# Kernel optimization log

Hardware: AMD Instinct MI355X
Metric: run time of the kernel (lower is better)

## Reference

```python
import jax, jax.numpy as jnp
import numpy as np

H = 512  # hidden_dimension
B = 32
S = 2048


def setup_inputs() -> dict:
    key = jax.random.key(0)
    k1, k2, k3, k4, k5, k6 = jax.random.split(key, 6)
    decoder_hide = jax.random.normal(k1, (B, H), dtype=jnp.float32)
    encoder_out = jax.random.normal(k2, (B, S, 2 * H), dtype=jnp.float32)
    mask = jax.random.randint(k3, (B, S), 0, 2, dtype=jnp.int32)
    bound = 1.0 / np.sqrt(3 * H)
    W_attn = jax.random.uniform(k4, (3 * H, H), minval=-bound, maxval=bound, dtype=jnp.float32)
    b_attn = jax.random.uniform(k5, (H,), minval=-bound, maxval=bound, dtype=jnp.float32)
    bound_v = 1.0 / np.sqrt(H)
    v_w = jax.random.uniform(k6, (H,), minval=-bound_v, maxval=bound_v, dtype=jnp.float32)
    return {"decoder_hide": decoder_hide, "encoder_out": encoder_out, "mask": mask,
            "W_attn": W_attn, "b_attn": b_attn, "v_w": v_w}


def reference(decoder_hide, encoder_out, mask, W_attn, b_attn, v_w):
    # Split the concat-linear: cat((h, enc)) @ W == h @ W[:H] + enc @ W[H:]
    W_h = W_attn[:H]        # [H, H]
    W_e = W_attn[H:]        # [2H, H]
    dec_proj = decoder_hide @ W_h + b_attn                 # [B, H]
    enc_proj = jnp.einsum('bse,eh->bsh', encoder_out, W_e)  # [B, S, H]
    energy = jnp.tanh(enc_proj + dec_proj[:, None, :])      # [B, S, H]
    attention = jnp.einsum('bsh,h->bs', energy, v_w)        # [B, S]
    attention = jnp.where(mask == 0, jnp.float32(-100000.0), attention)
    return jax.nn.softmax(attention, axis=1)
```

## Files before the change

### kernel.cpp

```cpp
#include <hip/hip_runtime.h>
#include <hip/hip_bf16.h>
#include <math.h>

#define Hdim 512
#define Bdim 32
#define Sdim 2048
#define Kdim 1024
#define Mtot (Bdim * Sdim)

#define RGROWS 64
#define HK 512
#define NSTEP 8
#define RGPB 4

typedef __attribute__((ext_vector_type(8))) short short8;
typedef __attribute__((ext_vector_type(4))) float floatx4;

__device__ __forceinline__ short f2bf(float f) {
    union { float f; unsigned u; } v; v.f = f;
    unsigned r = v.u + 0x7fffu + ((v.u >> 16) & 1u);
    return (short)(r >> 16);
}

__device__ __forceinline__ short8 cvt8(float4 a, float4 b) {
    union { short8 s; __hip_bfloat162 h[4]; } u;
    u.h[0] = __float22bfloat162_rn(make_float2(a.x, a.y));
    u.h[1] = __float22bfloat162_rn(make_float2(a.z, a.w));
    u.h[2] = __float22bfloat162_rn(make_float2(b.x, b.y));
    u.h[3] = __float22bfloat162_rn(make_float2(b.z, b.w));
    return u.s;
}

__device__ __forceinline__ float fast_tanh(float x) {
    float ax = fabsf(x);
    float e  = __expf(-2.0f * ax);
    float r  = (1.0f - e) * __builtin_amdgcn_rcpf(1.0f + e);
    return copysignf(r, x);
}

__global__ __launch_bounds__(256) void prep_kernel(
    const float* __restrict__ W_attn, const float* __restrict__ dec,
    const float* __restrict__ b_attn, short* __restrict__ Wbp,
    float* __restrict__ dec_proj)
{
    const int t = threadIdx.x;
    if (blockIdx.x < 512) {
        const float* We = W_attn + Hdim * Hdim;
        __shared__ short tile[32][33];
        const int k0 = (blockIdx.x >> 4) * 32;
        const int n0 = (blockIdx.x & 15) * 32;
        const int r = t >> 5, c = t & 31;
        #pragma unroll
        for (int rr = 0; rr < 4; ++rr)
            tile[r + rr * 8][c] = f2bf(We[(size_t)(k0 + r + rr * 8) * Hdim + n0 + c]);
        __syncthreads();
        if (t < 128) {
            const int n_loc = t >> 2;
            const int q     = t & 3;
            const int nt    = (n0 + n_loc) >> 4;
            const int lnn   = (n0 + n_loc) & 15;
            const int ks    = k0 >> 5;
            short8 v;
            #pragma unroll
            for (int r2 = 0; r2 < 8; ++r2) v[r2] = tile[q * 8 + r2][n_loc];
            ((short8*)Wbp)[((nt * 32 + ks) * 64) + q * 16 + lnn] = v;
        }
    } else {
        __shared__ float partl[2][128];
        const int bid = blockIdx.x - 512;
        const int b  = bid >> 2;
        const int cb = bid & 3;
        const int c  = cb * 128 + (t & 127);
        const int kh = t >> 7;
        float acc = 0.0f;
        const int kbeg = kh * 256, kend = kbeg + 256;
        #pragma unroll 8
        for (int k = kbeg; k < kend; ++k)
            acc = fmaf(dec[b * Hdim + k], W_attn[(size_t)k * Hdim + c], acc);
        partl[kh][t & 127] = acc;
        __syncthreads();
        if (t < 128)
            dec_proj[b * Hdim + cb * 128 + t] = partl[0][t] + partl[1][t] + b_attn[cb * 128 + t];
    }
}

__global__ __launch_bounds__(512, 2) void scores_kernel(
    const float* __restrict__ enc,
    const short* __restrict__ Wbp,
    const float* __restrict__ dec_proj,
    const float* __restrict__ v_w,
    float* __restrict__ scores)
{
    __shared__ __align__(16) short Abuf[2][RGROWS * HK];
    __shared__ float redl[RGROWS][9];

    const int t    = threadIdx.x;
    const int w    = t >> 6;
    const int lane = t & 63;
    const int ln   = lane & 15;
    const int quad = lane >> 4;

    const int b = blockIdx.x >> 3;
    const float* Ablk = enc + (size_t)blockIdx.x * (RGPB * RGROWS) * Kdim;

    const int pf0 = (quad ^ (ln & 7)) * 8;
    const int pf1 = pf0 ^ 32;

    const short8* Bp = ((const short8*)Wbp) + lane;

    float dpv[4], vwv[4];
    #pragma unroll
    for (int j = 0; j < 4; ++j) {
        const int col = w * 64 + j * 16 + ln;
        dpv[j] = dec_proj[b * Hdim + col];
        vwv[j] = v_w[col];
    }

    floatx4 acc[4][4];
    #pragma unroll
    for (int i = 0; i < 4; ++i)
        #pragma unroll
        for (int j = 0; j < 4; ++j)
            acc[i][j] = (floatx4)(0.0f);

    float4 stage[16];

    #define ISSUE(hh) do {                                                    \
        const float* p_ = Ablk + (size_t)((hh) >> 1) * RGROWS * Kdim          \
                         + ((hh) & 1) * HK + lane * 8;                        \
        _Pragma("unroll")                                                     \
        for (int j_ = 0; j_ < 8; ++j_) {                                      \
            const float4* g_ = (const float4*)(p_ + (size_t)(j_ * 8 + w) * Kdim); \
            stage[2 * j_]     = g_[0];                                        \
            stage[2 * j_ + 1] = g_[1];                                        \
        }                                                                     \
    } while (0)

    #define WRITEHALF(bi_) do {                                               \
        _Pragma("unroll")                                                     \
        for (int j_ = 0; j_ < 8; ++j_) {                                      \
            const int r_ = j_ * 8 + w;                                        \
            *(short8*)&Abuf[bi_][r_ * HK + ((lane ^ (r_ & 7)) << 3)] =        \
                cvt8(stage[2 * j_], stage[2 * j_ + 1]);                       \
        }                                                                     \
    } while (0)

    ISSUE(0);
    WRITEHALF(0);
    __syncthreads();

    #pragma unroll 1
    for (int h = 0; h < 2 * RGPB; ++h) {
        const int bi  = h & 1;
        const short* Ab = Abuf[bi];
        const int ksb = (h & 1) * 16;

        #pragma unroll
        for (int s = 0; s < NSTEP; ++s) {
            const int ks = ksb + 2 * s;
            short8 b0[4], b1[4];
            #pragma unroll
            for (int j = 0; j < 4; ++j)
                b0[j] = Bp[((size_t)(w * 4 + j) * 32 + ks) * 64];
            #pragma unroll
            for (int j = 0; j < 4; ++j)
                b1[j] = Bp[((size_t)(w * 4 + j) * 32 + ks + 1) * 64];

            if (s == 3 && h < 2 * RGPB - 1) ISSUE(h + 1);

            short8 af[4];
            #pragma unroll
            for (int i2 = 0; i2 < 4; ++i2)
                af[i2] = *(const short8*)&Ab[(i2 * 16 + ln) * HK + s * 64 + pf0];
            #pragma unroll
            for (int i2 = 0; i2 < 4; ++i2)
                #pragma unroll
                for (int j = 0; j < 4; ++j)
                    acc[i2][j] = __builtin_amdgcn_mfma_f32_16x16x32_bf16(
                                     af[i2], b0[j], acc[i2][j], 0, 0, 0);
            #pragma unroll
            for (int i2 = 0; i2 < 4; ++i2)
                af[i2] = *(const short8*)&Ab[(i2 * 16 + ln) * HK + s * 64 + pf1];
            #pragma unroll
            for (int i2 = 0; i2 < 4; ++i2)
                #pragma unroll
                for (int j = 0; j < 4; ++j)
                    acc[i2][j] = __builtin_amdgcn_mfma_f32_16x16x32_bf16(
                                     af[i2], b1[j], acc[i2][j], 0, 0, 0);
        }

        if (h & 1) {
            const int rg = h >> 1;
            #pragma unroll
            for (int i2 = 0; i2 < 4; ++i2) {
                #pragma unroll
                for (int reg = 0; reg < 4; ++reg) {
                    float s2 = 0.0f;
                    #pragma unroll
                    for (int j = 0; j < 4; ++j) {
                        float x = acc[i2][j][reg] + dpv[j];
                        s2 = fmaf(vwv[j], fast_tanh(x), s2);
                    }
                    s2 += __shfl_xor(s2, 1, 64);
                    s2 += __shfl_xor(s2, 2, 64);
                    s2 += __shfl_xor(s2, 4, 64);
                    s2 += __shfl_xor(s2, 8, 64);
                    if (ln == 0)
                        redl[i2 * 16 + quad * 4 + reg][w] = s2;
                }
            }
            __syncthreads();
            if (t < RGROWS) {
                float s2 = 0.0f;
                #pragma unroll
                for (int wv = 0; wv < 8; ++wv) s2 += redl[t][wv];
                scores[blockIdx.x * (RGPB * RGROWS) + rg * RGROWS + t] = s2;
            }
            #pragma unroll
            for (int i = 0; i < 4; ++i)
                #pragma unroll
                for (int j = 0; j < 4; ++j)
                    acc[i][j] = (floatx4)(0.0f);
        }

        if (h < 2 * RGPB - 1) WRITEHALF(bi ^ 1);
        __syncthreads();
    }
    #undef ISSUE
    #undef WRITEHALF
}

__global__ __launch_bounds__(256) void softmax_kernel(
    const float* __restrict__ scores, const int* __restrict__ mask,
    float* __restrict__ out)
{
    __shared__ float sred[8];
    const int b = blockIdx.x;
    const int t = threadIdx.x;
    const int lane = t & 63;
    const int wid  = t >> 6;

    float x[8];
    float m = -1e30f;
    #pragma unroll
    for (int j = 0; j < 8; ++j) {
        int idx = b * Sdim + j * 256 + t;
        float v = scores[idx];
        if (mask[idx] == 0) v = -100000.0f;
        x[j] = v;
        m = fmaxf(m, v);
    }
    #pragma unroll
    for (int off = 32; off >= 1; off >>= 1)
        m = fmaxf(m, __shfl_xor(m, off, 64));
    if (lane == 0) sred[wid] = m;
    __syncthreads();
    m = fmaxf(fmaxf(sred[0], sred[1]), fmaxf(sred[2], sred[3]));

    float s = 0.0f;
    #pragma unroll
    for (int j = 0; j < 8; ++j) {
        float e = __expf(x[j] - m);
        x[j] = e;
        s += e;
    }
    #pragma unroll
    for (int off = 32; off >= 1; off >>= 1)
        s += __shfl_xor(s, off, 64);
    if (lane == 0) sred[4 + wid] = s;
    __syncthreads();
    s = sred[4] + sred[5] + sred[6] + sred[7];

    const float inv = 1.0f / s;
    #pragma unroll
    for (int j = 0; j < 8; ++j)
        out[b * Sdim + j * 256 + t] = x[j] * inv;
}

extern "C" void kernel_launch(void* const* d_in, const int* in_sizes, int n_in,
                              void* d_out, int out_size, void* d_ws, size_t ws_size,
                              hipStream_t stream) {
    const float* dec  = (const float*)d_in[0];
    const float* enc  = (const float*)d_in[1];
    const int*   mask = (const int*)  d_in[2];
    const float* W    = (const float*)d_in[3];
    const float* ba   = (const float*)d_in[4];
    const float* vw   = (const float*)d_in[5];
    float* out = (float*)d_out;

    float* dec_proj = (float*)d_ws;
    short* Wbp      = (short*)(dec_proj + Bdim * Hdim);
    float* scores   = (float*)(Wbp + Hdim * Kdim);

    prep_kernel<<<640, 256, 0, stream>>>(W, dec, ba, Wbp, dec_proj);
    scores_kernel<<<Mtot / (RGPB * RGROWS), 512, 0, stream>>>(enc, Wbp, dec_proj, vw, scores);
    softmax_kernel<<<Bdim, 256, 0, stream>>>(scores, mask, out);
}
```

Baseline: 438.6 us.

## Warp-specialize scores kernel with dedicated producer waves for encoder staging

Adds four producer waves per block (768 threads) that load fp32 encoder rows, convert them to bf16 and write the swizzled LDS double buffer. The eight original waves now only do the MFMA loop and the tanh/v reduction. The aim is to take global-load latency and conversion work off the MFMA waves, so loads and matrix math run concurrently instead of being interleaved in one instruction stream. In exchange, fewer waves issue global loads (only a 4-deep per-wave prefetch), and the launch_bounds(768,3) hint may squeeze the register budget and cause spills.

```diff
diff --git a/kernel.cpp b/kernel.cpp
--- a/kernel.cpp
+++ b/kernel.cpp
@@ -84,7 +84,7 @@
     }
 }
 
-__global__ __launch_bounds__(512, 2) void scores_kernel(
+__global__ __launch_bounds__(768, 3) void scores_kernel(
     const float* __restrict__ enc,
     const short* __restrict__ Wbp,
     const float* __restrict__ dec_proj,
@@ -99,6 +99,8 @@
     const int lane = t & 63;
     const int ln   = lane & 15;
     const int quad = lane >> 4;
+    const bool is_prod = (w >= 8);
+    const int pw = w - 8;
 
     const int b = blockIdx.x >> 3;
     const float* Ablk = enc + (size_t)blockIdx.x * (RGPB * RGROWS) * Kdim;
@@ -109,11 +111,13 @@
     const short8* Bp = ((const short8*)Wbp) + lane;
 
     float dpv[4], vwv[4];
-    #pragma unroll
-    for (int j = 0; j < 4; ++j) {
-        const int col = w * 64 + j * 16 + ln;
-        dpv[j] = dec_proj[b * Hdim + col];
-        vwv[j] = v_w[col];
+    if (!is_prod) {
+        #pragma unroll
+        for (int j = 0; j < 4; ++j) {
+            const int col = w * 64 + j * 16 + ln;
+            dpv[j] = dec_proj[b * Hdim + col];
+            vwv[j] = v_w[col];
+        }
     }
 
     floatx4 acc[4][4];
@@ -123,90 +127,94 @@
         for (int j = 0; j < 4; ++j)
             acc[i][j] = (floatx4)(0.0f);
 
-    float4 stage[16];
-
-    #define ISSUE(hh) do {                                                    \
-        const float* p_ = Ablk + (size_t)((hh) >> 1) * RGROWS * Kdim          \
-                         + ((hh) & 1) * HK + lane * 8;                        \
+    #define STAGE(hh) do {                                                    \
+        const float* base_ = Ablk + (size_t)((hh) >> 1) * RGROWS * Kdim       \
+                            + ((hh) & 1) * HK;                                \
+        short* dst_ = Abuf[(hh) & 1];                                         \
+        float4 pa[4], pb[4];                                                  \
         _Pragma("unroll")                                                     \
-        for (int j_ = 0; j_ < 8; ++j_) {                                      \
-            const float4* g_ = (const float4*)(p_ + (size_t)(j_ * 8 + w) * Kdim); \
-            stage[2 * j_]     = g_[0];                                        \
-            stage[2 * j_ + 1] = g_[1];                                        \
+        for (int pr = 0; pr < 4; ++pr) {                                      \
+            const float4* g_ = (const float4*)(base_                          \
+                + (size_t)(pw * 16 + pr) * Kdim + lane * 8);                  \
+            pa[pr] = g_[0]; pb[pr] = g_[1];                                   \
+        }                                                                     \
+        _Pragma("unroll")                                                     \
+        for (int it = 0; it < 16; ++it) {                                     \
+            const int r_ = pw * 16 + it;                                      \
+            float4 a_ = pa[it & 3], b_ = pb[it & 3];                          \
+            if (it + 4 < 16) {                                                \
+                const float4* g_ = (const float4*)(base_                      \
+                    + (size_t)(r_ + 4) * Kdim + lane * 8);                    \
+                pa[it & 3] = g_[0]; pb[it & 3] = g_[1];                       \
+            }                                                                 \
+            *(short8*)&dst_[r_ * HK + ((lane ^ (r_ & 7)) << 3)] = cvt8(a_, b_); \
         }                                                                     \
     } while (0)
 
-    #define WRITEHALF(bi_) do {                                               \
-        _Pragma("unroll")                                                     \
-        for (int j_ = 0; j_ < 8; ++j_) {                                      \
-            const int r_ = j_ * 8 + w;                                        \
-            *(short8*)&Abuf[bi_][r_ * HK + ((lane ^ (r_ & 7)) << 3)] =        \
-                cvt8(stage[2 * j_], stage[2 * j_ + 1]);                       \
-        }                                                                     \
-    } while (0)
-
-    ISSUE(0);
-    WRITEHALF(0);
+    if (is_prod) STAGE(0);
     __syncthreads();
 
     #pragma unroll 1
     for (int h = 0; h < 2 * RGPB; ++h) {
-        const int bi  = h & 1;
-        const short* Ab = Abuf[bi];
-        const int ksb = (h & 1) * 16;
-
-        #pragma unroll
-        for (int s = 0; s < NSTEP; ++s) {
-            const int ks = ksb + 2 * s;
-            short8 b0[4], b1[4];
+        const int bi = h & 1;
+
+        if (!is_prod) {
+            const short* Ab = Abuf[bi];
+            const int ksb = bi * 16;
             #pragma unroll
-            for (int j = 0; j < 4; ++j)
-                b0[j] = Bp[((size_t)(w * 4 + j) * 32 + ks) * 64];
-            #pragma unroll
-            for (int j = 0; j < 4; ++j)
-                b1[j] = Bp[((size_t)(w * 4 + j) * 32 + ks + 1) * 64];
-
-            if (s == 3 && h < 2 * RGPB - 1) ISSUE(h + 1);
-
-            short8 af[4];
-            #pragma unroll
-            for (int i2 = 0; i2 < 4; ++i2)
-                af[i2] = *(const short8*)&Ab[(i2 * 16 + ln) * HK + s * 64 + pf0];
-            #pragma unroll
-            for (int i2 = 0; i2 < 4; ++i2)
+            for (int s = 0; s < NSTEP; ++s) {
+                const int ks = ksb + 2 * s;
+                short8 bc[8];
                 #pragma unroll
                 for (int j = 0; j < 4; ++j)
-                    acc[i2][j] = __builtin_amdgcn_mfma_f32_16x16x32_bf16(
-                                     af[i2], b0[j], acc[i2][j], 0, 0, 0);
-            #pragma unroll
-            for (int i2 = 0; i2 < 4; ++i2)
-                af[i2] = *(const short8*)&Ab[(i2 * 16 + ln) * HK + s * 64 + pf1];
-            #pragma unroll
-            for (int i2 = 0; i2 < 4; ++i2)
+                    bc[j] = Bp[((size_t)(w * 4 + j) * 32 + ks) * 64];
                 #pragma unroll
                 for (int j = 0; j < 4; ++j)
-                    acc[i2][j] = __builtin_amdgcn_mfma_f32_16x16x32_bf16(
-                                     af[i2], b1[j], acc[i2][j], 0, 0, 0);
+                    bc[4 + j] = Bp[((size_t)(w * 4 + j) * 32 + ks + 1) * 64];
+
+                short8 af[4];
+                #pragma unroll
+                for (int i2 = 0; i2 < 4; ++i2)
+                    af[i2] = *(const short8*)&Ab[(i2 * 16 + ln) * HK + s * 64 + pf0];
+                #pragma unroll
+                for (int i2 = 0; i2 < 4; ++i2)
+                    #pragma unroll
+                    for (int j = 0; j < 4; ++j)
+                        acc[i2][j] = __builtin_amdgcn_mfma_f32_16x16x32_bf16(
+                                         af[i2], bc[j], acc[i2][j], 0, 0, 0);
+                #pragma unroll
+                for (int i2 = 0; i2 < 4; ++i2)
+                    af[i2] = *(const short8*)&Ab[(i2 * 16 + ln) * HK + s * 64 + pf1];
+                #pragma unroll
+                for (int i2 = 0; i2 < 4; ++i2)
+                    #pragma unroll
+                    for (int j = 0; j < 4; ++j)
+                        acc[i2][j] = __builtin_amdgcn_mfma_f32_16x16x32_bf16(
+                                         af[i2], bc[4 + j], acc[i2][j], 0, 0, 0);
+            }
+        } else {
+            if (h + 1 < 2 * RGPB) STAGE(h + 1);
         }
 
         if (h & 1) {
-            const int rg = h >> 1;
-            #pragma unroll
-            for (int i2 = 0; i2 < 4; ++i2) {
-                #pragma unroll
-                for (int reg = 0; reg < 4; ++reg) {
-                    float s2 = 0.0f;
+            if (!is_prod) {
+                #pragma unroll
+                for (int i2 = 0; i2 < 4; ++i2) {
                     #pragma unroll
-                    for (int j = 0; j < 4; ++j) {
-                        float x = acc[i2][j][reg] + dpv[j];
-                        s2 = fmaf(vwv[j], fast_tanh(x), s2);
+                    for (int reg = 0; reg < 4; ++reg) {
+                        float s2 = 0.0f;
+                        #pragma unroll
+                        for (int j = 0; j < 4; ++j) {
+                            float x = acc[i2][j][reg] + dpv[j];
+                            s2 = fmaf(vwv[j], fast_tanh(x), s2);
+                        }
+                        s2 += __shfl_xor(s2, 1, 64);
+                        s2 += __shfl_xor(s2, 2, 64);
+                        s2 += __shfl_xor(s2, 4, 64);
+                        s2 += __shfl_xor(s2, 8, 64);
+                        if (ln == 0)
+                            redl[i2 * 16 + quad * 4 + reg][w] = s2;
                     }
-                    s2 += __shfl_xor(s2, 1, 64);
-                    s2 += __shfl_xor(s2, 2, 64);
-                    s2 += __shfl_xor(s2, 4, 64);
-                    s2 += __shfl_xor(s2, 8, 64);
-                    if (ln == 0)
-                        redl[i2 * 16 + quad * 4 + reg][w] = s2;
                 }
             }
             __syncthreads();
@@ -214,20 +222,20 @@
                 float s2 = 0.0f;
                 #pragma unroll
                 for (int wv = 0; wv < 8; ++wv) s2 += redl[t][wv];
-                scores[blockIdx.x * (RGPB * RGROWS) + rg * RGROWS + t] = s2;
+                scores[blockIdx.x * (RGPB * RGROWS) + (h >> 1) * RGROWS + t] = s2;
             }
-            #pragma unroll
-            for (int i = 0; i < 4; ++i)
-                #pragma unroll
-                for (int j = 0; j < 4; ++j)
-                    acc[i][j] = (floatx4)(0.0f);
+            if (!is_prod) {
+                #pragma unroll
+                for (int i = 0; i < 4; ++i)
+                    #pragma unroll
+                    for (int j = 0; j < 4; ++j)
+                        acc[i][j] = (floatx4)(0.0f);
+            }
         }
 
-        if (h < 2 * RGPB - 1) WRITEHALF(bi ^ 1);
         __syncthreads();
     }
-    #undef ISSUE
-    #undef WRITEHALF
+    #undef STAGE
 }
 
 __global__ __launch_bounds__(256) void softmax_kernel(
@@ -293,6 +301,6 @@
     float* scores   = (float*)(Wbp + Hdim * Kdim);
 
     prep_kernel<<<640, 256, 0, stream>>>(W, dec, ba, Wbp, dec_proj);
-    scores_kernel<<<Mtot / (RGPB * RGROWS), 512, 0, stream>>>(enc, Wbp, dec_proj, vw, scores);
+    scores_kernel<<<Mtot / (RGPB * RGROWS), 768, 0, stream>>>(enc, Wbp, dec_proj, vw, scores);
     softmax_kernel<<<Bdim, 256, 0, stream>>>(scores, mask, out);
 }
```

New measurement: 447.8 us. +2.1%, slower.
